# Kernel optimization log

Hardware: AMD Instinct MI355X
Metric: run time of the kernel (lower is better)

## Reference

```python
import jax, jax.numpy as jnp
import numpy as np

R = 4        # in_transformations == out_transformations
FS = 3       # filter_size
PAD = 1
STRIDE = 1


def setup_inputs() -> dict:
    key = jax.random.key(0)
    k1, k2, k3 = jax.random.split(key, 3)
    B, Cin, O, K = 16, 64, 64, 4
    Ctot = Cin * R  # 256
    x = jax.random.normal(k1, (B, Ctot, 64, 64), dtype=jnp.float32)
    # kernel bank: [num_dynamic_kernels, out_channels, in_channels, f, f]
    kernel_bank = jax.random.normal(k2, (K, O, Cin, FS, FS), dtype=jnp.float32) * 0.05
    # routing fc: Linear(total_in_channels -> num_kernels)
    fc_w = jax.random.normal(k3, (K, Ctot), dtype=jnp.float32) * 0.05
    fc_b = jnp.zeros((K,), dtype=jnp.float32)
    return {"x": x, "kernel_bank": kernel_bank, "fc_w": fc_w, "fc_b": fc_b}


def reference(x, kernel_bank, fc_w, fc_b):
    B, Ctot, H, W = x.shape
    K, O, Cin, f, _ = kernel_bank.shape
    # --- dynamic routing: global avg pool -> fc -> sigmoid ---
    pooled = x.mean(axis=(2, 3))                                  # [B, Ctot]
    coeffs = jax.nn.sigmoid(pooled @ fc_w.T + fc_b)               # [B, K]
    # --- per-sample kernel synthesis ---
    base = jnp.einsum('bk,kocij->bocij', coeffs, kernel_bank)     # [B, O, Cin, f, f]
    # rotations rot90^k for k in 0..R-1 (matches torch.rot90 dims=(-2,-1))
    rotated = jnp.stack([jnp.rot90(base, k, axes=(-2, -1)) for k in range(R)], axis=1)  # [B, R, O, Cin, f, f]
    # block kernel: block (r_out, r_in) uses rotation index (r_out - r_in) % R,
    # so the r_in sum of convs becomes one conv over all R*Cin input channels.
    r_out = jnp.arange(R)[:, None]
    r_in = jnp.arange(R)[None, :]
    idx = (r_out - r_in) % R                                      # [R, R]
    big = rotated[:, idx]                                         # [B, R_out, R_in, O, Cin, f, f]
    big = big.transpose(0, 1, 3, 2, 4, 5, 6).reshape(B, R * O, R * Cin, f, f)
    # --- per-sample conv (vmapped over batch; each sample has its own kernel) ---
    def conv_one(xi, wi):
        return jax.lax.conv_general_dilated(
            xi[None], wi,
            window_strides=(STRIDE, STRIDE),
            padding=[(PAD, PAD), (PAD, PAD)],
            dimension_numbers=('NCHW', 'OIHW', 'NCHW'))[0]
    return jax.vmap(conv_one)(x, big)                             # [B, R*O, H, W]
```

## Files before the change

### kernel.cpp

```cpp
#include <hip/hip_runtime.h>
#include <hip/hip_bf16.h>
#include <math.h>

#define BATCH 16
#define CT    256
#define HW    64
#define OCH   64
#define NK    4
#define HP    66
#define NPIX  4356

typedef __attribute__((ext_vector_type(4))) float  f32x4;
typedef __attribute__((ext_vector_type(8))) short  s16x8;
typedef __attribute__((ext_vector_type(4))) unsigned short u16x4;

#define GLOBAL_AS __attribute__((address_space(1)))
#define LDS_AS    __attribute__((address_space(3)))

__device__ __constant__ int c_rotsrc[4][9] = {
    {0,1,2,3,4,5,6,7,8},
    {2,5,8,1,4,7,0,3,6},
    {8,7,6,5,4,3,2,1,0},
    {6,3,0,7,4,1,8,5,2}
};

static __device__ inline unsigned short f2bf(float f) {
    union { __hip_bfloat16 h; unsigned short u; } cv;
    cv.h = __float2bfloat16(f);
    return cv.u;
}

__global__ __launch_bounds__(256) void xpose_pool(const float* __restrict__ x,
                                                  unsigned short* __restrict__ xTg,
                                                  float* __restrict__ partial) {
    const int ci0 = blockIdx.x * 64;
    const int g0  = ci0 >> 3;
    const int pr  = blockIdx.y;
    const int b   = blockIdx.z;
    const int t   = threadIdx.x;

    if (pr == 0 || pr == HP-1) {
        for (int u = t; u < 8*HP; u += 256) {
            int g = u / HP, c = u % HP;
            *(s16x8*)(xTg + ((((size_t)(b*32 + g0 + g))*NPIX) + pr*HP + c)*8) =
                (s16x8)(short)0;
        }
        return;
    }
    const int r = pr - 1;

    __shared__ unsigned short tile[64][70];
    const int cilH = t >> 4;
    const int c0   = (t & 15) * 4;
    #pragma unroll
    for (int i = 0; i < 4; ++i) {
        int cil = cilH + i*16;
        f32x4 v = *(const f32x4*)(x + (((size_t)(b*CT + ci0 + cil))*HW + r)*HW + c0);
        tile[cil][c0+0] = f2bf(v[0]);
        tile[cil][c0+1] = f2bf(v[1]);
        tile[cil][c0+2] = f2bf(v[2]);
        tile[cil][c0+3] = f2bf(v[3]);
        float s = v[0] + v[1] + v[2] + v[3];
        s += __shfl_xor(s, 1, 16);
        s += __shfl_xor(s, 2, 16);
        s += __shfl_xor(s, 4, 16);
        s += __shfl_xor(s, 8, 16);
        if ((t & 15) == 0)
            partial[((size_t)(b*HW) + r)*CT + ci0 + cil] = s;
    }
    __syncthreads();

    if (t < 16) {
        int g = t & 7, side = t >> 3;
        *(s16x8*)(xTg + ((((size_t)(b*32 + g0 + g))*NPIX) + pr*HP + side*(HP-1))*8) =
            (s16x8)(short)0;
    }
    #pragma unroll
    for (int i = 0; i < 4; ++i) {
        int u = i*256 + t;
        int c = u & 63, cil0 = (u >> 6) * 4;
        u16x4 w;
        w[0] = tile[cil0+0][c];
        w[1] = tile[cil0+1][c];
        w[2] = tile[cil0+2][c];
        w[3] = tile[cil0+3][c];
        *(u16x4*)(xTg + ((((size_t)(b*32 + g0 + (cil0>>3)))*NPIX) + pr*HP + c + 1)*8
                  + (cil0 & 4)) = w;
    }
}

__global__ __launch_bounds__(256) void coeff_kernel(const float* __restrict__ partial,
                                                    const float* __restrict__ fc_w,
                                                    const float* __restrict__ fc_b,
                                                    float* __restrict__ coeffs) {
    const int b = blockIdx.x;
    const int t = threadIdx.x;
    const float* pp = partial + (size_t)b*HW*CT + t;
    float s = 0.f;
    #pragma unroll 8
    for (int r = 0; r < HW; ++r) s += pp[(size_t)r*CT];
    __shared__ float pool[CT];
    pool[t] = s * (1.f / (HW*HW));
    __syncthreads();
    const int w = t >> 6, l = t & 63;
    float d = 0.f;
    for (int c = l; c < CT; c += 64) d += pool[c] * fc_w[w*CT + c];
    for (int off = 32; off; off >>= 1) d += __shfl_down(d, off, 64);
    if (l == 0)
        coeffs[b*NK + w] = 1.f / (1.f + expf(-(d + fc_b[w])));
}

__global__ __launch_bounds__(256) void bankrot_kernel(const float* __restrict__ bank,
                                                      float* __restrict__ P) {
    const int idx = blockIdx.x * 256 + threadIdx.x;
    const int o = idx & 63;
    const int c = (idx >> 6) & 63;
    const int k = idx >> 12;
    const float* bp = bank + ((size_t)((k*OCH + o)*64 + c))*9;
    float v[9];
    #pragma unroll
    for (int s = 0; s < 9; ++s) v[s] = bp[s];
    #pragma unroll
    for (int rr = 0; rr < 4; ++rr)
        #pragma unroll
        for (int s = 0; s < 9; ++s)
            P[(size_t)(((k*4 + rr)*9 + s))*4096 + c*64 + o] = v[c_rotsrc[rr][s]];
}

__global__ __launch_bounds__(256) void wbuild_kernel(const float* __restrict__ coeffs,
                                                     const float* __restrict__ P,
                                                     unsigned short* __restrict__ Wb) {
    const int cig = blockIdx.x;
    const int s   = blockIdx.y;
    const int co  = threadIdx.x;
    const int ro  = co >> 6;
    const int o   = co & 63;
    const int ri  = cig >> 3;
    const int rr  = (ro - ri) & 3;
    const int c8  = (cig & 7) * 8;

    float r[NK][8];
    #pragma unroll
    for (int k = 0; k < NK; ++k) {
        const float* pp = P + (size_t)(((k*4 + rr)*9 + s))*4096 + o;
        #pragma unroll
        for (int q = 0; q < 8; ++q)
            r[k][q] = pp[(c8 + q)*64];
    }
    #pragma unroll
    for (int b = 0; b < BATCH; ++b) {
        const float cf0 = coeffs[b*NK+0], cf1 = coeffs[b*NK+1];
        const float cf2 = coeffs[b*NK+2], cf3 = coeffs[b*NK+3];
        s16x8 w;
        #pragma unroll
        for (int q = 0; q < 8; ++q) {
            float v = cf0*r[0][q] + cf1*r[1][q] + cf2*r[2][q] + cf3*r[3][q];
            w[q] = (short)f2bf(v);
        }
        *(s16x8*)(Wb + ((((size_t)(b*9 + s)*32 + cig)*256 + co) << 3)) = w;
    }
}

#define CHUNK_UNITS 1056
#define BUF_UNITS   1088
__global__ __launch_bounds__(256, 2) void conv_mfma(
        const unsigned short* __restrict__ xTg,
        const unsigned short* __restrict__ Wb,
        float* __restrict__ out) {
    const int bid = blockIdx.x;
    const int b   = (bid & 7)*2 + ((bid >> 3) & 1);
    const int rt  = bid >> 4;
    const int r0  = rt * 2;

    const int t    = threadIdx.x;
    const int w    = t >> 6;
    const int lane = t & 63;
    const int lo16 = lane & 15;
    const int hi4  = lane >> 4;

    __shared__ __align__(16) unsigned short Xs[2*BUF_UNITS*8];

    f32x4 acc[4][8];
    #pragma unroll
    for (int f = 0; f < 4; ++f)
        #pragma unroll
        for (int p = 0; p < 8; ++p)
            acc[f][p] = (f32x4)0.f;

#define STAGE(CH, BUF)                                                          \
    do {                                                                        \
        _Pragma("unroll")                                                       \
        for (int it = 0; it < 5; ++it) {                                        \
            int ubase = it*256 + w*64;                                          \
            if (ubase < CHUNK_UNITS) {                                          \
                int u  = ubase + lane;                                          \
                int us = u > (CHUNK_UNITS-1) ? (CHUNK_UNITS-1) : u;             \
                int q  = us / 264;                                              \
                int pl = us - q*264;                                            \
                const unsigned short* src = xTg +                               \
                    (((size_t)(b*32 + (CH)*4 + q))*NPIX + r0*HP + pl)*8;        \
                __builtin_amdgcn_global_load_lds(                               \
                    (const GLOBAL_AS void*)src,                                 \
                    (LDS_AS void*)(Xs + (size_t)((BUF)*BUF_UNITS + ubase)*8),   \
                    16, 0, 0);                                                  \
            }                                                                   \
        }                                                                       \
    } while (0)

    STAGE(0, 0);

    for (int ch = 0; ch < 8; ++ch) {
        __syncthreads();
        if (ch < 7) STAGE(ch+1, (ch+1) & 1);
        const char* Xb = (const char*)Xs + (ch & 1)*(BUF_UNITS*16)
                         + hi4*(264*16) + lo16*16;

        #pragma unroll
        for (int s = 0; s < 9; ++s) {
            const int dr = s / 3, dc = s % 3;
            const unsigned short* wp = Wb +
                ((((size_t)(b*9 + s)*32) + ch*4 + hi4)*256 + w*64 + lo16)*8;
            s16x8 a0 = *(const s16x8*)(wp + 0*128);
            s16x8 a1 = *(const s16x8*)(wp + 1*128);
            s16x8 a2 = *(const s16x8*)(wp + 2*128);
            s16x8 a3 = *(const s16x8*)(wp + 3*128);
            #pragma unroll
            for (int p = 0; p < 8; ++p) {
                const int pixbase = ((p >> 2) + dr)*HP + dc + (p & 3)*16;
                s16x8 bf = *(const s16x8*)(Xb + pixbase*16);
                acc[0][p] = __builtin_amdgcn_mfma_f32_16x16x32_bf16(a0, bf, acc[0][p], 0, 0, 0);
                acc[1][p] = __builtin_amdgcn_mfma_f32_16x16x32_bf16(a1, bf, acc[1][p], 0, 0, 0);
                acc[2][p] = __builtin_amdgcn_mfma_f32_16x16x32_bf16(a2, bf, acc[2][p], 0, 0, 0);
                acc[3][p] = __builtin_amdgcn_mfma_f32_16x16x32_bf16(a3, bf, acc[3][p], 0, 0, 0);
            }
        }
    }
#undef STAGE

    #pragma unroll
    for (int f = 0; f < 4; ++f)
        #pragma unroll
        for (int p = 0; p < 8; ++p) {
            const int row = r0 + (p >> 2);
            const int colb = (p & 3)*16 + lo16;
            #pragma unroll
            for (int j = 0; j < 4; ++j) {
                int co = w*64 + f*16 + hi4*4 + j;
                out[(((size_t)(b*CT + co))*HW + row)*HW + colb] = acc[f][p][j];
            }
        }
}

extern "C" void kernel_launch(void* const* d_in, const int* in_sizes, int n_in,
                              void* d_out, int out_size, void* d_ws, size_t ws_size,
                              hipStream_t stream) {
    const float* x    = (const float*)d_in[0];
    const float* bank = (const float*)d_in[1];
    const float* fc_w = (const float*)d_in[2];
    const float* fc_b = (const float*)d_in[3];
    float* out = (float*)d_out;

    char* wsb = (char*)d_ws;
    float* partial = (float*)wsb;
    float* Prot    = (float*)wsb;
    float* coeffs  = (float*)(wsb + 2359296);
    unsigned short* Wb  = (unsigned short*)(wsb + 2360320);
    unsigned short* xTg = (unsigned short*)(wsb + 21234688);

    xpose_pool<<<dim3(4, HP, BATCH), 256, 0, stream>>>(x, xTg, partial);
    coeff_kernel<<<BATCH, 256, 0, stream>>>(partial, fc_w, fc_b, coeffs);
    bankrot_kernel<<<64, 256, 0, stream>>>(bank, Prot);
    wbuild_kernel<<<dim3(32, 9), 256, 0, stream>>>(coeffs, Prot, Wb);
    conv_mfma<<<512, 256, 0, stream>>>(xTg, Wb, out);
}
```

Baseline: 100.2 us.

## Double-buffer weight fragments in registers and interleave LDS staging with MFMA phases

```diff
diff --git a/kernel.cpp b/kernel.cpp
--- a/kernel.cpp
+++ b/kernel.cpp
@@ -161,16 +161,18 @@
     }
 }
 
-#define CHUNK_UNITS 1056
-#define BUF_UNITS   1088
+#define SLAB_U  266
+#define CHUNK_U 1064
+#define BUF_U   1088
+#define MF(A_, B_, C_) __builtin_amdgcn_mfma_f32_16x16x32_bf16(A_, B_, C_, 0, 0, 0)
+
 __global__ __launch_bounds__(256, 2) void conv_mfma(
         const unsigned short* __restrict__ xTg,
         const unsigned short* __restrict__ Wb,
         float* __restrict__ out) {
     const int bid = blockIdx.x;
     const int b   = (bid & 7)*2 + ((bid >> 3) & 1);
-    const int rt  = bid >> 4;
-    const int r0  = rt * 2;
+    const int r0  = (bid >> 4) * 2;
 
     const int t    = threadIdx.x;
     const int w    = t >> 6;
@@ -178,7 +180,7 @@
     const int lo16 = lane & 15;
     const int hi4  = lane >> 4;
 
-    __shared__ __align__(16) unsigned short Xs[2*BUF_UNITS*8];
+    __shared__ __align__(16) unsigned short Xs[2*BUF_U*8];
 
     f32x4 acc[4][8];
     #pragma unroll
@@ -187,55 +189,93 @@
         for (int p = 0; p < 8; ++p)
             acc[f][p] = (f32x4)0.f;
 
-#define STAGE(CH, BUF)                                                          \
+    s16x8 Aa[3][4], Ab[3][4];
+
+#define LOAD_A(DST, CH, SBASE)                                                  \
     do {                                                                        \
         _Pragma("unroll")                                                       \
-        for (int it = 0; it < 5; ++it) {                                        \
+        for (int si = 0; si < 3; ++si) {                                        \
+            const unsigned short* wp = Wb +                                     \
+                ((((size_t)(b*9 + (SBASE) + si)*32) + (CH)*4 + hi4)*256         \
+                 + w*64 + lo16)*8;                                              \
+            _Pragma("unroll")                                                   \
+            for (int f = 0; f < 4; ++f)                                         \
+                DST[si][f] = *(const s16x8*)(wp + f*128);                       \
+        }                                                                       \
+    } while (0)
+
+#define STAGE_R(CH, BUF, IT0, IT1)                                              \
+    do {                                                                        \
+        _Pragma("unroll")                                                       \
+        for (int it = (IT0); it < (IT1); ++it) {                                \
             int ubase = it*256 + w*64;                                          \
-            if (ubase < CHUNK_UNITS) {                                          \
+            if (ubase < CHUNK_U) {                                              \
                 int u  = ubase + lane;                                          \
-                int us = u > (CHUNK_UNITS-1) ? (CHUNK_UNITS-1) : u;             \
-                int q  = us / 264;                                              \
-                int pl = us - q*264;                                            \
+                int us = u > (CHUNK_U-1) ? (CHUNK_U-1) : u;                     \
+                int q  = us / SLAB_U;                                           \
+                int pl = us - q*SLAB_U;                                         \
                 const unsigned short* src = xTg +                               \
                     (((size_t)(b*32 + (CH)*4 + q))*NPIX + r0*HP + pl)*8;        \
                 __builtin_amdgcn_global_load_lds(                               \
                     (const GLOBAL_AS void*)src,                                 \
-                    (LDS_AS void*)(Xs + (size_t)((BUF)*BUF_UNITS + ubase)*8),   \
+                    (LDS_AS void*)(Xs + (size_t)((BUF)*BUF_U + ubase)*8),       \
                     16, 0, 0);                                                  \
             }                                                                   \
         }                                                                       \
     } while (0)
 
-    STAGE(0, 0);
-
-    for (int ch = 0; ch < 8; ++ch) {
-        __syncthreads();
-        if (ch < 7) STAGE(ch+1, (ch+1) & 1);
-        const char* Xb = (const char*)Xs + (ch & 1)*(BUF_UNITS*16)
-                         + hi4*(264*16) + lo16*16;
-
-        #pragma unroll
-        for (int s = 0; s < 9; ++s) {
-            const int dr = s / 3, dc = s % 3;
-            const unsigned short* wp = Wb +
-                ((((size_t)(b*9 + s)*32) + ch*4 + hi4)*256 + w*64 + lo16)*8;
-            s16x8 a0 = *(const s16x8*)(wp + 0*128);
-            s16x8 a1 = *(const s16x8*)(wp + 1*128);
-            s16x8 a2 = *(const s16x8*)(wp + 2*128);
-            s16x8 a3 = *(const s16x8*)(wp + 3*128);
-            #pragma unroll
-            for (int p = 0; p < 8; ++p) {
-                const int pixbase = ((p >> 2) + dr)*HP + dc + (p & 3)*16;
-                s16x8 bf = *(const s16x8*)(Xb + pixbase*16);
-                acc[0][p] = __builtin_amdgcn_mfma_f32_16x16x32_bf16(a0, bf, acc[0][p], 0, 0, 0);
-                acc[1][p] = __builtin_amdgcn_mfma_f32_16x16x32_bf16(a1, bf, acc[1][p], 0, 0, 0);
-                acc[2][p] = __builtin_amdgcn_mfma_f32_16x16x32_bf16(a2, bf, acc[2][p], 0, 0, 0);
-                acc[3][p] = __builtin_amdgcn_mfma_f32_16x16x32_bf16(a3, bf, acc[3][p], 0, 0, 0);
-            }
-        }
-    }
-#undef STAGE
+#define MFMA_PHASE(ASET, SBASE, XB)                                             \
+    do {                                                                        \
+        __builtin_amdgcn_s_setprio(1);                                          \
+        _Pragma("unroll")                                                       \
+        for (int si = 0; si < 3; ++si) {                                        \
+            const int s_ = (SBASE) + si, dr = s_/3, dc = s_%3;                  \
+            _Pragma("unroll")                                                   \
+            for (int p = 0; p < 8; ++p) {                                       \
+                const int pixbase = ((p>>2) + dr)*HP + dc + (p&3)*16;           \
+                s16x8 bf = *(const s16x8*)((XB) + pixbase*16);                  \
+                acc[0][p] = MF(ASET[si][0], bf, acc[0][p]);                     \
+                acc[1][p] = MF(ASET[si][1], bf, acc[1][p]);                     \
+                acc[2][p] = MF(ASET[si][2], bf, acc[2][p]);                     \
+                acc[3][p] = MF(ASET[si][3], bf, acc[3][p]);                     \
+            }                                                                   \
+        }                                                                       \
+        __builtin_amdgcn_s_setprio(0);                                          \
+    } while (0)
+
+#define CHUNK(CH, AC, AO)                                                       \
+    do {                                                                        \
+        const char* Xb = (const char*)Xs + ((CH)&1)*(BUF_U*16)                  \
+                         + hi4*(SLAB_U*16) + lo16*16;                           \
+        LOAD_A(AO, CH, 3);                                                      \
+        __builtin_amdgcn_sched_barrier(0);                                      \
+        if ((CH) < 7) STAGE_R((CH)+1, ((CH)+1)&1, 0, 3);                        \
+        __builtin_amdgcn_sched_barrier(0);                                      \
+        MFMA_PHASE(AC, 0, Xb);                                                  \
+        LOAD_A(AC, CH, 6);                                                      \
+        __builtin_amdgcn_sched_barrier(0);                                      \
+        if ((CH) < 7) STAGE_R((CH)+1, ((CH)+1)&1, 3, 5);                        \
+        __builtin_amdgcn_sched_barrier(0);                                      \
+        MFMA_PHASE(AO, 3, Xb);                                                  \
+        LOAD_A(AO, ((CH) < 7 ? (CH)+1 : 0), 0);                                 \
+        __builtin_amdgcn_sched_barrier(0);                                      \
+        MFMA_PHASE(AC, 6, Xb);                                                  \
+        __syncthreads();                                                        \
+    } while (0)
+
+    STAGE_R(0, 0, 0, 5);
+    LOAD_A(Aa, 0, 0);
+    __syncthreads();
+
+    for (int cc = 0; cc < 8; cc += 2) {
+        CHUNK(cc,   Aa, Ab);
+        CHUNK(cc+1, Ab, Aa);
+    }
+
+#undef CHUNK
+#undef MFMA_PHASE
+#undef STAGE_R
+#undef LOAD_A
 
     #pragma unroll
     for (int f = 0; f < 4; ++f)
```

Measured after the change: 123.0 us. +22.8%, slower.
